# Performance work log

Measured on AMD Instinct MI355X. Metric: run time of the kernel, lower is better.

## Reference

```python
import jax, jax.numpy as jnp
import numpy as np

N, E = 20000, 320000
IN_DIM, EDGE_DIM, HID = 64, 16, 64
# (in_c, heads, channels, out_c) per layer; last layer heads=1, concat=False
DIMS = [(64, 4, 64, 256), (256, 4, 64, 256), (256, 1, 64, 64)]


def _ln(x, g, b):
    m = x.mean(-1, keepdims=True)
    v = x.var(-1, keepdims=True)
    return (x - m) / jnp.sqrt(v + 1e-5) * g + b


def _gatv2(x, ei, ea, Wl, bl, Wr, br, We, att, bc, concat):
    # PyG GATv2Conv, eval mode (no dropout), add_self_loops=True, fill_value='mean'
    n = x.shape[0]
    H, C = att.shape
    ar = jnp.arange(n, dtype=ei.dtype)
    src = jnp.concatenate([ei[0], ar])
    dst = jnp.concatenate([ei[1], ar])
    ea_f = jnp.concatenate([ea, jnp.broadcast_to(ea.mean(0), (n, ea.shape[1]))], 0)
    xl = (x @ Wl + bl).reshape(n, H, C)   # source transform
    xr = (x @ Wr + br).reshape(n, H, C)   # target transform
    ee = (ea_f @ We).reshape(-1, H, C)    # edge transform (no bias in PyG)
    e = jax.nn.leaky_relu(xl[src] + xr[dst] + ee, 0.2)       # [E+N, H, C]
    score = jnp.einsum('ehc,hc->eh', e, att)                 # [E+N, H]
    mx = jax.ops.segment_max(score, dst, num_segments=n)
    a = jnp.exp(score - mx[dst])
    a = a / (jax.ops.segment_sum(a, dst, num_segments=n)[dst] + 1e-16)
    out = jax.ops.segment_sum(a[:, :, None] * xl[src], dst, num_segments=n)  # [N,H,C]
    out = out.reshape(n, H * C) if concat else out.mean(1)
    return out + bc


def _forward(x, eis, eas, Wp, bp, gp, bep, layers):
    h = jax.nn.gelu(_ln(x @ Wp + bp, gp, bep), approximate=False)
    for i in range(3):
        Wl, bl, Wr, br, We, att, bc, g, be, Wsk, bsk = layers[i]
        res = h @ Wsk + bsk
        h = _gatv2(h, eis[i], eas[i], Wl, bl, Wr, br, We, att, bc, i < 2)
        h = jax.nn.gelu(_ln(h, g, be), approximate=False) + res
    return h


def setup_inputs() -> dict:
    key = jax.random.key(0)
    ks = iter(jax.random.split(key, 64))
    rn = lambda shape, s=0.05: jax.random.normal(next(ks), shape, jnp.float32) * s
    d = {'x': jax.random.normal(next(ks), (N, IN_DIM), jnp.float32)}
    for i in range(3):
        d['ei%d' % i] = jax.random.randint(next(ks), (2, E), 0, N, jnp.int32)
        d['ea%d' % i] = jax.random.normal(next(ks), (E, EDGE_DIM), jnp.float32)
    d['Wp'] = rn((IN_DIM, HID)); d['bp'] = jnp.zeros(HID)
    d['gp'] = jnp.ones(HID); d['bep'] = jnp.zeros(HID)
    for i, (ic, H, C, oc) in enumerate(DIMS):
        hc = H * C
        d['Wl%d' % i] = rn((ic, hc)); d['bl%d' % i] = jnp.zeros(hc)
        d['Wr%d' % i] = rn((ic, hc)); d['br%d' % i] = jnp.zeros(hc)
        d['We%d' % i] = rn((EDGE_DIM, hc))
        d['att%d' % i] = rn((H, C), 0.1)
        d['bc%d' % i] = jnp.zeros(hc if i < 2 else C)
        d['g%d' % i] = jnp.ones(oc); d['be%d' % i] = jnp.zeros(oc)
        d['Wsk%d' % i] = rn((ic, oc)); d['bsk%d' % i] = jnp.zeros(oc)
    return d


def reference(x, ei0, ea0, ei1, ea1, ei2, ea2, Wp, bp, gp, bep,
              Wl0, bl0, Wr0, br0, We0, att0, bc0, g0, be0, Wsk0, bsk0,
              Wl1, bl1, Wr1, br1, We1, att1, bc1, g1, be1, Wsk1, bsk1,
              Wl2, bl2, Wr2, br2, We2, att2, bc2, g2, be2, Wsk2, bsk2):
    layers = [
        (Wl0, bl0, Wr0, br0, We0, att0, bc0, g0, be0, Wsk0, bsk0),
        (Wl1, bl1, Wr1, br1, We1, att1, bc1, g1, be1, Wsk1, bsk1),
        (Wl2, bl2, Wr2, br2, We2, att2, bc2, g2, be2, Wsk2, bsk2),
    ]
    return _forward(x, (ei0, ei1, ei2), (ea0, ea1, ea2), Wp, bp, gp, bep, layers)
```

## Files before the change

### kernel.cpp

```cpp
#include <hip/hip_runtime.h>
#include <hip/hip_bf16.h>
#include <math.h>

#define NV 20000
#define NE 320000
#define CSR_PAD 8

typedef __attribute__((ext_vector_type(8))) short bf16x8;
typedef __attribute__((ext_vector_type(4))) float f32x4;
typedef __attribute__((ext_vector_type(2))) _Float16 h2;

static __device__ __forceinline__ ushort f2b(float f) {
  __hip_bfloat16 h = __float2bfloat16(f);
  return *reinterpret_cast<ushort*>(&h);
}
static __device__ __forceinline__ float b2f(ushort u) {
  union { ushort s[2]; float f; } c;
  c.s[0] = 0; c.s[1] = u;
  return c.f;
}
static __device__ __forceinline__ ushort f2h(float f) {
  _Float16 h = (_Float16)f;
  return *reinterpret_cast<ushort*>(&h);
}
static __device__ __forceinline__ float blo(unsigned u) { return __uint_as_float(u << 16); }
static __device__ __forceinline__ float bhi(unsigned u) { return __uint_as_float(u & 0xffff0000u); }

static __device__ __forceinline__ float wave_sum64(float x) {
  x += __int_as_float(__builtin_amdgcn_update_dpp(0, __float_as_int(x), 0x111, 0xF, 0xF, true));
  x += __int_as_float(__builtin_amdgcn_update_dpp(0, __float_as_int(x), 0x112, 0xF, 0xF, true));
  x += __int_as_float(__builtin_amdgcn_update_dpp(0, __float_as_int(x), 0x114, 0xF, 0xF, true));
  x += __int_as_float(__builtin_amdgcn_update_dpp(0, __float_as_int(x), 0x118, 0xF, 0xF, true));
  x += __int_as_float(__builtin_amdgcn_update_dpp(0, __float_as_int(x), 0x142, 0xA, 0xF, true));
  x += __int_as_float(__builtin_amdgcn_update_dpp(0, __float_as_int(x), 0x143, 0xC, 0xF, true));
  return __int_as_float(__builtin_amdgcn_readlane(__float_as_int(x), 63));
}

static __device__ __forceinline__ float sum16(float x) {
  x += __int_as_float(__builtin_amdgcn_update_dpp(0, __float_as_int(x), 0x121, 0xF, 0xF, true));
  x += __int_as_float(__builtin_amdgcn_update_dpp(0, __float_as_int(x), 0x122, 0xF, 0xF, true));
  x += __int_as_float(__builtin_amdgcn_update_dpp(0, __float_as_int(x), 0x124, 0xF, 0xF, true));
  x += __int_as_float(__builtin_amdgcn_update_dpp(0, __float_as_int(x), 0x128, 0xF, 0xF, true));
  return x;
}

static __device__ __forceinline__ float dot16h(const uint4* __restrict__ E,
                                               const h2* __restrict__ Wch) {
#if __has_builtin(__builtin_amdgcn_fdot2)
  const h2* e = (const h2*)E;
  float s = 0.f;
#pragma unroll
  for (int j = 0; j < 8; ++j) s = __builtin_amdgcn_fdot2(e[j], Wch[j], s, false);
  return s;
#else
  const unsigned* u = (const unsigned*)E;
  float s = 0.f;
#pragma unroll
  for (int j = 0; j < 8; ++j) {
    union { unsigned v; h2 h; } cv; cv.v = u[j];
    s = fmaf((float)cv.h[0], (float)Wch[j][0], s);
    s = fmaf((float)cv.h[1], (float)Wch[j][1], s);
  }
  return s;
#endif
}

struct CJob { const float* src; ushort* dst; int K, M; };
struct PrepArgs {
  const int* ei[3];
  const float* ea[3];
  int* counts[3];
  float* easum[3];
  CJob jobs[9];
  const float *x, *Wp, *bp, *gp, *bep;
  ushort* h0;
};

__global__ __launch_bounds__(256) void prep_kernel(PrepArgs a) {
  const int y = blockIdx.y, t = threadIdx.x;
  if (y < 3) {
    if (blockIdx.x < 256) {
      const float4* ea4 = (const float4*)a.ea[y];
      const int cg = t & 3;
      int r = blockIdx.x * 64 + (t >> 2);
      const int rstride = 256 * 64;
      float4 s = make_float4(0.f, 0.f, 0.f, 0.f);
      for (; r < NE; r += rstride) {
        float4 v = ea4[(size_t)r * 4 + cg];
        s.x += v.x; s.y += v.y; s.z += v.z; s.w += v.w;
      }
      __shared__ float4 red4[256];
      red4[t] = s;
      __syncthreads();
      if (t < 4) {
        float4 tot = make_float4(0.f, 0.f, 0.f, 0.f);
        for (int j = t; j < 256; j += 4) {
          float4 v = red4[j];
          tot.x += v.x; tot.y += v.y; tot.z += v.z; tot.w += v.w;
        }
        atomicAdd(&a.easum[y][t * 4 + 0], tot.x);
        atomicAdd(&a.easum[y][t * 4 + 1], tot.y);
        atomicAdd(&a.easum[y][t * 4 + 2], tot.z);
        atomicAdd(&a.easum[y][t * 4 + 3], tot.w);
      }
    }
    int i = blockIdx.x * 256 + t;
    if (i < NE) atomicAdd(&a.counts[y][a.ei[y][NE + i]], 1);
  } else if (y == 3) {
#pragma unroll
    for (int j = 0; j < 9; ++j) {
      CJob jb = a.jobs[j];
      const int total = jb.M * jb.K;
      for (int i = blockIdx.x * 256 + t; i < total; i += gridDim.x * 256) {
        int m = i / jb.K, k = i - m * jb.K;
        jb.dst[i] = f2b(jb.src[(size_t)k * jb.M + m]);
      }
    }
  } else {
    int wid = t >> 6, lane = t & 63;
    for (int row = blockIdx.x * 4 + wid; row < NV; row += gridDim.x * 4) {
      float xv = a.x[(size_t)row * 64 + lane];
      float acc = a.bp[lane];
#pragma unroll
      for (int k = 0; k < 64; ++k) {
        float v = __shfl(xv, k, 64);
        acc = fmaf(v, a.Wp[k * 64 + lane], acc);
      }
      float s1 = wave_sum64(acc), s2 = wave_sum64(acc * acc);
      float mean = s1 * (1.0f / 64.0f);
      float var  = s2 * (1.0f / 64.0f) - mean * mean;
      float yv = (acc - mean) * rsqrtf(var + 1e-5f) * a.gp[lane] + a.bep[lane];
      float gel = 0.5f * yv * (1.0f + erff(yv * 0.70710678118654752f));
      a.h0[(size_t)row * 64 + lane] = f2b(gel);
    }
  }
}

__global__ __launch_bounds__(1024) void scan_kernel(
    int* __restrict__ countsA, int* __restrict__ cursorA)
{
  int* counts = countsA + blockIdx.x * (NV + 1);
  int* cursor = cursorA + blockIdx.x * NV;
  __shared__ int ws[16];
  __shared__ int wexcl[17];
  const int t = threadIdx.x, lane = t & 63, wid = t >> 6;
  const int base = t * 20;
  int v[20];
  int tot = 0;
#pragma unroll
  for (int j = 0; j < 20; ++j) {
    int i = base + j;
    v[j] = (i < NV) ? counts[i] : 0;
    tot += v[j];
  }
  int x = tot;
#pragma unroll
  for (int o = 1; o < 64; o <<= 1) {
    int yy = __shfl_up(x, o, 64);
    if (lane >= o) x += yy;
  }
  if (lane == 63) ws[wid] = x;
  __syncthreads();
  if (t == 0) {
    int r = 0;
#pragma unroll
    for (int j = 0; j < 16; ++j) { wexcl[j] = r; r += ws[j]; }
    wexcl[16] = r;
  }
  __syncthreads();
  int run = wexcl[wid] + (x - tot);
#pragma unroll
  for (int j = 0; j < 20; ++j) {
    int i = base + j;
    if (i < NV) { counts[i] = run; cursor[i] = run; }
    run += v[j];
  }
  if (t == 0) counts[NV] = wexcl[16];
}

struct G0SArgs {
  const ushort *A, *WT;
  const float *b0, *b1, *b2;
  ushort *O0, *O1; float* O2;
  int K, M1, M2, Mtot, NT;
  const int* ei[3]; const float* ea[3];
  int* cursor;
  unsigned* csr[3]; ushort* eab[3]; int HC[3];
};

__global__ __launch_bounds__(256) void gemm0_scatter_kernel(G0SArgs a) {
  __shared__ ushort As[128][40];
  __shared__ ushort Bs[64][40];
  const int t = threadIdx.x;
  if ((int)blockIdx.x < a.NT) {
    const int wave = t >> 6, lane = t & 63;
    const int mcols = a.Mtot >> 6;
    const int col0 = ((int)blockIdx.x % mcols) * 64, row0 = ((int)blockIdx.x / mcols) * 128;
    const int m_ = lane & 15, q = lane >> 4;
    f32x4 acc[2][4];
#pragma unroll
    for (int i = 0; i < 2; ++i)
#pragma unroll
      for (int j = 0; j < 4; ++j) acc[i][j] = (f32x4){0.f, 0.f, 0.f, 0.f};
    const int ar = t >> 1, ac = (t & 1) * 16;
    const int br = t >> 2, bcol = (t & 3) * 8;
    const ushort* Ap = a.A + (size_t)(row0 + ar) * a.K + ac;
    const ushort* Bp = a.WT + (size_t)(col0 + br) * a.K + bcol;
    const bool a_ok = (row0 + ar) < NV;
    for (int k0 = 0; k0 < a.K; k0 += 32) {
      uint4 av0 = make_uint4(0, 0, 0, 0), av1 = make_uint4(0, 0, 0, 0);
      if (a_ok) { av0 = *(const uint4*)(Ap + k0); av1 = *(const uint4*)(Ap + k0 + 8); }
      uint4 bv = *(const uint4*)(Bp + k0);
      *(uint4*)&As[ar][ac] = av0;
      *(uint4*)&As[ar][ac + 8] = av1;
      *(uint4*)&Bs[br][bcol] = bv;
      __syncthreads();
      bf16x8 a0 = *(const bf16x8*)&As[wave * 32 + m_][q * 8];
      bf16x8 a1 = *(const bf16x8*)&As[wave * 32 + 16 + m_][q * 8];
#pragma unroll
      for (int cf = 0; cf < 4; ++cf) {
        bf16x8 b = *(const bf16x8*)&Bs[cf * 16 + m_][q * 8];
        acc[0][cf] = __builtin_amdgcn_mfma_f32_16x16x32_bf16(a0, b, acc[0][cf], 0, 0, 0);
        acc[1][cf] = __builtin_amdgcn_mfma_f32_16x16x32_bf16(a1, b, acc[1][cf], 0, 0, 0);
      }
      __syncthreads();
    }
    const float* bias; int base, mode, Wd;
    if (col0 < a.M1)      { bias = a.b0; base = 0;    mode = 0; Wd = a.M1; }
    else if (col0 < a.M2) { bias = a.b1; base = a.M1; mode = 1; Wd = a.M2 - a.M1; }
    else                  { bias = a.b2; base = a.M2; mode = 2; Wd = a.Mtot - a.M2; }
#pragma unroll
    for (int rf = 0; rf < 2; ++rf) {
#pragma unroll
      for (int cf = 0; cf < 4; ++cf) {
        int col = col0 + cf * 16 + m_ - base;
        float bb = bias[col];
#pragma unroll
        for (int r = 0; r < 4; ++r) {
          int row = row0 + wave * 32 + rf * 16 + q * 4 + r;
          if (row < NV) {
            float v = acc[rf][cf][r] + bb;
            if (mode == 0)      a.O0[(size_t)row * Wd + col] = f2b(v);
            else if (mode == 1) a.O1[(size_t)row * Wd + col] = f2b(v);
            else                a.O2[(size_t)row * Wd + col] = v;
          }
        }
      }
    }
  } else {
    const int per = NE + CSR_PAD;
    int gi = ((int)blockIdx.x - a.NT) * 256 + t;
    if (gi >= 3 * per) return;
    int l = gi / per, i = gi - l * per;
    if (i >= NE) {
      a.csr[l][i] = 0u;
      uint4 z = make_uint4(0, 0, 0, 0);
      *(uint4*)(a.eab[l] + (size_t)i * 16) = z;
      *(uint4*)(a.eab[l] + (size_t)i * 16 + 8) = z;
      return;
    }
    int dst = a.ei[l][NE + i], src = a.ei[l][i];
    int pos = atomicAdd(&a.cursor[(size_t)l * NV + dst], 1);
    a.csr[l][pos] = (unsigned)(src * a.HC[l]);
    const float4* er = (const float4*)(a.ea[l] + (size_t)i * 16);
    float4 q0 = er[0], q1 = er[1], q2 = er[2], q3 = er[3];
    uint4 w0, w1;
    w0.x = (unsigned)f2h(q0.x) | ((unsigned)f2h(q0.y) << 16);
    w0.y = (unsigned)f2h(q0.z) | ((unsigned)f2h(q0.w) << 16);
    w0.z = (unsigned)f2h(q1.x) | ((unsigned)f2h(q1.y) << 16);
    w0.w = (unsigned)f2h(q1.z) | ((unsigned)f2h(q1.w) << 16);
    w1.x = (unsigned)f2h(q2.x) | ((unsigned)f2h(q2.y) << 16);
    w1.y = (unsigned)f2h(q2.z) | ((unsigned)f2h(q2.w) << 16);
    w1.z = (unsigned)f2h(q3.x) | ((unsigned)f2h(q3.y) << 16);
    w1.w = (unsigned)f2h(q3.z) | ((unsigned)f2h(q3.w) << 16);
    *(uint4*)(a.eab[l] + (size_t)pos * 16) = w0;
    *(uint4*)(a.eab[l] + (size_t)pos * 16 + 8) = w1;
  }
}

__global__ __launch_bounds__(256) void gemm_fused(
    const ushort* __restrict__ A, const ushort* __restrict__ WT,
    const float* __restrict__ b0, const float* __restrict__ b1,
    const float* __restrict__ b2,
    ushort* __restrict__ O0, ushort* __restrict__ O1, float* __restrict__ O2,
    int N, int K, int M1, int M2, int Mtot)
{
  __shared__ ushort As[128][40];
  __shared__ ushort Bs[64][40];
  const int t = threadIdx.x, wave = t >> 6, lane = t & 63;
  const int row0 = blockIdx.y * 128, col0 = blockIdx.x * 64;
  const int m_ = lane & 15, q = lane >> 4;
  f32x4 acc[2][4];
#pragma unroll
  for (int i = 0; i < 2; ++i)
#pragma unroll
    for (int j = 0; j < 4; ++j) acc[i][j] = (f32x4){0.f, 0.f, 0.f, 0.f};
  const int ar = t >> 1, ac = (t & 1) * 16;
  const int br = t >> 2, bcol = (t & 3) * 8;
  const ushort* Ap = A + (size_t)(row0 + ar) * K + ac;
  const ushort* Bp = WT + (size_t)(col0 + br) * K + bcol;
  const bool a_ok = (row0 + ar) < N;
  for (int k0 = 0; k0 < K; k0 += 32) {
    uint4 av0 = make_uint4(0, 0, 0, 0), av1 = make_uint4(0, 0, 0, 0);
    if (a_ok) { av0 = *(const uint4*)(Ap + k0); av1 = *(const uint4*)(Ap + k0 + 8); }
    uint4 bv = *(const uint4*)(Bp + k0);
    *(uint4*)&As[ar][ac] = av0;
    *(uint4*)&As[ar][ac + 8] = av1;
    *(uint4*)&Bs[br][bcol] = bv;
    __syncthreads();
    bf16x8 a0 = *(const bf16x8*)&As[wave * 32 + m_][q * 8];
    bf16x8 a1 = *(const bf16x8*)&As[wave * 32 + 16 + m_][q * 8];
#pragma unroll
    for (int cf = 0; cf < 4; ++cf) {
      bf16x8 b = *(const bf16x8*)&Bs[cf * 16 + m_][q * 8];
      acc[0][cf] = __builtin_amdgcn_mfma_f32_16x16x32_bf16(a0, b, acc[0][cf], 0, 0, 0);
      acc[1][cf] = __builtin_amdgcn_mfma_f32_16x16x32_bf16(a1, b, acc[1][cf], 0, 0, 0);
    }
    __syncthreads();
  }
  const float* bias; int base, mode, Wd;
  if (col0 < M1)      { bias = b0; base = 0;  mode = 0; Wd = M1; }
  else if (col0 < M2) { bias = b1; base = M1; mode = 1; Wd = M2 - M1; }
  else                { bias = b2; base = M2; mode = 2; Wd = Mtot - M2; }
#pragma unroll
  for (int rf = 0; rf < 2; ++rf) {
#pragma unroll
    for (int cf = 0; cf < 4; ++cf) {
      int col = col0 + cf * 16 + m_ - base;
      float bb = bias[col];
#pragma unroll
      for (int r = 0; r < 4; ++r) {
        int row = row0 + wave * 32 + rf * 16 + q * 4 + r;
        if (row < N) {
          float v = acc[rf][cf][r] + bb;
          if (mode == 0)      O0[(size_t)row * Wd + col] = f2b(v);
          else if (mode == 1) O1[(size_t)row * Wd + col] = f2b(v);
          else                O2[(size_t)row * Wd + col] = v;
        }
      }
    }
  }
}

__global__ __launch_bounds__(256) void agg4_kernel(
    const ushort* __restrict__ eab, const float* __restrict__ easum,
    const float* __restrict__ We,
    const ushort* __restrict__ xl, const ushort* __restrict__ xr,
    const float* __restrict__ att, const float* __restrict__ bc,
    const float* __restrict__ g, const float* __restrict__ be,
    const float* __restrict__ res,
    const int* __restrict__ offs, const unsigned* __restrict__ csr,
    ushort* __restrict__ houtb, int E)
{
  const int t = threadIdx.x, lane = t & 63, wave = t >> 6;
  const int n = blockIdx.x * 4 + wave;
  const int cb = 4 * lane;
  const size_t rowb = (size_t)n * 256 + cb;
  const float L2E = 1.4426950408889634f;

  float4 atv = *(const float4*)(att + cb);
  float at[4] = {atv.x * L2E, atv.y * L2E, atv.z * L2E, atv.w * L2E};

  h2 Wch[4][8];
  float esf[4] = {0.f, 0.f, 0.f, 0.f};
#pragma unroll
  for (int k = 0; k < 8; ++k) {
    float4 wr0 = *(const float4*)(We + (2 * k) * 256 + cb);
    float4 wr1 = *(const float4*)(We + (2 * k + 1) * 256 + cb);
    const float* w0 = &wr0.x;
    const float* w1 = &wr1.x;
    float e0 = easum[2 * k], e1 = easum[2 * k + 1];
#pragma unroll
    for (int j = 0; j < 4; ++j) {
      esf[j] = fmaf(e0, w0[j], esf[j]);
      esf[j] = fmaf(e1, w1[j], esf[j]);
      Wch[j][k] = (h2){(_Float16)w0[j], (_Float16)w1[j]};
    }
  }
#pragma unroll
  for (int j = 0; j < 4; ++j) esf[j] *= 1.0f / (float)E;

  uint2 qr = *(const uint2*)(xr + rowb);
  float xrv[4] = {blo(qr.x), bhi(qr.x), blo(qr.y), bhi(qr.y)};
  uint2 qn = *(const uint2*)(xl + rowb);
  float xln[4] = {blo(qn.x), bhi(qn.x), blo(qn.y), bhi(qn.y)};

  float p = 0.f;
#pragma unroll
  for (int j = 0; j < 4; ++j) {
    float v = xln[j] + xrv[j] + esf[j];
    v = v > 0.f ? v : 0.2f * v;
    p = fmaf(v, at[j], p);
  }
  float wself = exp2f(sum16(p));
  float acc[4];
#pragma unroll
  for (int j = 0; j < 4; ++j) acc[j] = wself * xln[j];
  float denom = wself;

  const int beg = __builtin_amdgcn_readfirstlane(offs[n]);
  const int end = __builtin_amdgcn_readfirstlane(offs[n + 1]);

  unsigned P[2];
  uint4 EA[2][2];
  uint2 XL[2];
#pragma unroll
  for (int k = 0; k < 2; ++k) {
    P[k] = csr[beg + k];
    const uint4* ep = (const uint4*)(eab + (size_t)(beg + k) * 16);
    EA[k][0] = ep[0]; EA[k][1] = ep[1];
  }
#pragma unroll
  for (int k = 0; k < 2; ++k)
    XL[k] = *(const uint2*)(xl + __builtin_amdgcn_readfirstlane(P[k]) + cb);

  for (int idx = beg; idx < end; idx += 2) {
    unsigned Q[2];
    uint4 EB[2][2];
    uint2 XN[2];
#pragma unroll
    for (int k = 0; k < 2; ++k) Q[k] = csr[idx + 2 + k];
#pragma unroll
    for (int k = 0; k < 2; ++k) {
      const uint4* ep = (const uint4*)(eab + (size_t)(idx + 2 + k) * 16);
      EB[k][0] = ep[0]; EB[k][1] = ep[1];
    }
#pragma unroll
    for (int k = 0; k < 2; ++k)
      XN[k] = *(const uint2*)(xl + __builtin_amdgcn_readfirstlane(Q[k]) + cb);

#pragma unroll
    for (int k = 0; k < 2; ++k) {
      float xf[4] = {blo(XL[k].x), bhi(XL[k].x), blo(XL[k].y), bhi(XL[k].y)};
      float pp = 0.f;
#pragma unroll
      for (int j = 0; j < 4; ++j) {
        float ee = dot16h(EA[k], Wch[j]);
        float v = xf[j] + xrv[j] + ee;
        v = v > 0.f ? v : 0.2f * v;
        pp = fmaf(v, at[j], pp);
      }
      float S = sum16(pp);
      float w = (idx + k < end) ? exp2f(S) : 0.f;
#pragma unroll
      for (int j = 0; j < 4; ++j) acc[j] = fmaf(w, xf[j], acc[j]);
      denom += w;
    }
#pragma unroll
    for (int k = 0; k < 2; ++k) { P[k] = Q[k]; EA[k][0] = EB[k][0]; EA[k][1] = EB[k][1]; XL[k] = XN[k]; }
  }

  const float inv = 1.0f / (denom + 1e-16f);
  float4 bcv = *(const float4*)(bc + cb);
  float out[4];
  out[0] = acc[0] * inv + bcv.x; out[1] = acc[1] * inv + bcv.y;
  out[2] = acc[2] * inv + bcv.z; out[3] = acc[3] * inv + bcv.w;

  float so1 = out[0] + out[1] + out[2] + out[3];
  float so2 = out[0] * out[0] + out[1] * out[1] + out[2] * out[2] + out[3] * out[3];
  float s1 = wave_sum64(so1), s2 = wave_sum64(so2);
  float mean = s1 * (1.0f / 256.0f);
  float var  = s2 * (1.0f / 256.0f) - mean * mean;
  float rstd = rsqrtf(var + 1e-5f);
  float4 gv = *(const float4*)(g + cb);
  float4 bev = *(const float4*)(be + cb);
  float4 rv = *(const float4*)(res + rowb);
  const float* gp = &gv.x; const float* bep = &bev.x; const float* rp = &rv.x;
  ushort ob[4];
#pragma unroll
  for (int j = 0; j < 4; ++j) {
    float y = (out[j] - mean) * rstd * gp[j] + bep[j];
    float gel = 0.5f * y * (1.0f + erff(y * 0.70710678118654752f));
    ob[j] = f2b(gel + rp[j]);
  }
  uint2 ov;
  ov.x = (unsigned)ob[0] | ((unsigned)ob[1] << 16);
  ov.y = (unsigned)ob[2] | ((unsigned)ob[3] << 16);
  *(uint2*)(houtb + rowb) = ov;
}

__global__ __launch_bounds__(256, 4) void agg1_kernel(
    const ushort* __restrict__ eab, const float* __restrict__ easum,
    const float* __restrict__ We,
    const ushort* __restrict__ xl, const ushort* __restrict__ xr,
    const float* __restrict__ att, const float* __restrict__ bc,
    const float* __restrict__ g, const float* __restrict__ be,
    const float* __restrict__ res,
    const int* __restrict__ offs, const unsigned* __restrict__ csr,
    float* __restrict__ houtf, int E)
{
  const int HC = 64;
  const int t = threadIdx.x, lane = t & 63, wave = t >> 6;
  const int n = blockIdx.x * 4 + wave;
  const int c = lane;

  const float xr_t = b2f(xr[(size_t)n * HC + c]);
  const float att_t = att[c] * 1.4426950408889634f;
  float eself = 0.f;
  h2 Wch[8];
#pragma unroll
  for (int j = 0; j < 8; ++j) {
    float w0 = We[(2 * j) * HC + c], w1 = We[(2 * j + 1) * HC + c];
    eself = fmaf(easum[2 * j], w0, eself);
    eself = fmaf(easum[2 * j + 1], w1, eself);
    Wch[j] = (h2){(_Float16)w0, (_Float16)w1};
  }
  eself *= 1.0f / (float)E;

  const float xln = b2f(xl[(size_t)n * HC + c]);
  float vs = xln + xr_t + eself;
  vs = vs > 0.f ? vs : 0.2f * vs;
  const float wself = exp2f(wave_sum64(vs * att_t));
  float acc = wself * xln, denom = wself;

  const int beg = __builtin_amdgcn_readfirstlane(offs[n]);
  const int end = __builtin_amdgcn_readfirstlane(offs[n + 1]);

  unsigned P[4];
  uint4 EA[4][2];
  float XL[4];
#pragma unroll
  for (int k = 0; k < 4; ++k) {
    P[k] = csr[beg + k];
    const uint4* ep = (const uint4*)(eab + (size_t)(beg + k) * 16);
    EA[k][0] = ep[0]; EA[k][1] = ep[1];
  }
#pragma unroll
  for (int k = 0; k < 4; ++k)
    XL[k] = b2f(xl[__builtin_amdgcn_readfirstlane(P[k]) + c]);

  for (int idx = beg; idx < end; idx += 4) {
    unsigned Q[4];
    uint4 EB[4][2];
    float XLN[4];
#pragma unroll
    for (int k = 0; k < 4; ++k) Q[k] = csr[idx + 4 + k];
#pragma unroll
    for (int k = 0; k < 4; ++k) {
      const uint4* ep = (const uint4*)(eab + (size_t)(idx + 4 + k) * 16);
      EB[k][0] = ep[0]; EB[k][1] = ep[1];
    }
#pragma unroll
    for (int k = 0; k < 4; ++k)
      XLN[k] = b2f(xl[__builtin_amdgcn_readfirstlane(Q[k]) + c]);

    float wv[4];
#pragma unroll
    for (int k = 0; k < 4; ++k) {
      float ee = dot16h(EA[k], Wch);
      float v = XL[k] + xr_t + ee;
      v = v > 0.f ? v : 0.2f * v;
      float S = wave_sum64(v * att_t);
      wv[k] = (idx + k < end) ? exp2f(S) : 0.f;
    }
#pragma unroll
    for (int k = 0; k < 4; ++k) { acc = fmaf(wv[k], XL[k], acc); denom += wv[k]; }
#pragma unroll
    for (int k = 0; k < 4; ++k) {
      P[k] = Q[k]; EA[k][0] = EB[k][0]; EA[k][1] = EB[k][1]; XL[k] = XLN[k];
    }
  }

  float out = acc / (denom + 1e-16f) + bc[c];
  float s1 = wave_sum64(out), s2 = wave_sum64(out * out);
  float mean = s1 / (float)HC;
  float var  = s2 / (float)HC - mean * mean;
  float y = (out - mean) * rsqrtf(var + 1e-5f) * g[c] + be[c];
  float gel = 0.5f * y * (1.0f + erff(y * 0.70710678118654752f));
  houtf[(size_t)n * HC + c] = gel + res[(size_t)n * HC + c];
}

extern "C" void kernel_launch(void* const* d_in, const int* in_sizes, int n_in,
                              void* d_out, int out_size, void* d_ws, size_t ws_size,
                              hipStream_t stream)
{
  auto in = [&](int i) { return (const float*)d_in[i]; };

  const int ic[3] = {64, 256, 256}, hc[3] = {256, 256, 64}, oc[3] = {256, 256, 64};
  const int CSRN = NE + CSR_PAD;

  char* w = (char*)d_ws;
  size_t off = 0;
  auto alloc = [&](size_t bytes) { void* p = w + off; off = (off + bytes + 511) & ~(size_t)511; return p; };
  ushort* B1   = (ushort*)alloc((size_t)NV * 256 * 2);
  ushort* B2   = (ushort*)alloc((size_t)NV * 256 * 2);
  float*  B3   = (float*)alloc((size_t)NV * 256 * 4);
  ushort* h0bf = (ushort*)alloc((size_t)NV * 64 * 2);
  ushort* h1bf = (ushort*)alloc((size_t)NV * 256 * 2);
  ushort* h2bf = (ushort*)alloc((size_t)NV * 256 * 2);
  ushort* Wcat[3];
  for (int i = 0; i < 3; ++i)
    Wcat[i] = (ushort*)alloc((size_t)(2 * hc[i] + oc[i]) * ic[i] * 2);
  float*    easumA  = (float*)alloc(3 * 64);
  int*      countsA = (int*)alloc((size_t)3 * (NV + 1) * 4);
  int*      cursorA = (int*)alloc((size_t)3 * NV * 4);
  unsigned* csrA    = (unsigned*)alloc((size_t)3 * CSRN * 4);
  ushort*   eabA    = (ushort*)alloc((size_t)3 * CSRN * 16 * 2);

  hipMemsetAsync(easumA, 0, 512 + (size_t)3 * (NV + 1) * 4, stream);

  PrepArgs pa;
  for (int i = 0; i < 3; ++i) {
    pa.ei[i] = (const int*)d_in[1 + 2 * i];
    pa.ea[i] = in(2 + 2 * i);
    pa.counts[i] = countsA + i * (NV + 1);
    pa.easum[i] = easumA + i * 16;
    pa.jobs[i * 3 + 0] = {in(11 + 11 * i), Wcat[i],                             ic[i], hc[i]};
    pa.jobs[i * 3 + 1] = {in(13 + 11 * i), Wcat[i] + (size_t)hc[i] * ic[i],     ic[i], hc[i]};
    pa.jobs[i * 3 + 2] = {in(20 + 11 * i), Wcat[i] + (size_t)2 * hc[i] * ic[i], ic[i], oc[i]};
  }
  pa.x = in(0); pa.Wp = in(7); pa.bp = in(8); pa.gp = in(9); pa.bep = in(10);
  pa.h0 = h0bf;
  prep_kernel<<<dim3(1344, 5), 256, 0, stream>>>(pa);

  scan_kernel<<<3, 1024, 0, stream>>>(countsA, cursorA);

  G0SArgs ga;
  ga.A = h0bf; ga.WT = Wcat[0];
  ga.b0 = in(12); ga.b1 = in(14); ga.b2 = in(21);
  ga.O0 = B1; ga.O1 = B2; ga.O2 = B3;
  ga.K = 64; ga.M1 = 256; ga.M2 = 512; ga.Mtot = 768;
  ga.NT = (768 / 64) * ((NV + 127) / 128);
  for (int i = 0; i < 3; ++i) {
    ga.ei[i] = (const int*)d_in[1 + 2 * i];
    ga.ea[i] = in(2 + 2 * i);
    ga.csr[i] = csrA + (size_t)i * CSRN;
    ga.eab[i] = eabA + (size_t)i * CSRN * 16;
    ga.HC[i] = hc[i];
  }
  ga.cursor = cursorA;
  const int scat_blocks = (3 * (NE + CSR_PAD) + 255) / 256;
  gemm0_scatter_kernel<<<ga.NT + scat_blocks, 256, 0, stream>>>(ga);

  agg4_kernel<<<NV / 4, 256, 0, stream>>>(
      eabA + 0, easumA + 0, in(15), B1, B2, in(16), in(17), in(18), in(19),
      B3, countsA, csrA, h1bf, NE);

  gemm_fused<<<dim3(768 / 64, (NV + 127) / 128), 256, 0, stream>>>(
      h1bf, Wcat[1], in(23), in(25), in(32), B1, B2, B3, NV, 256, 256, 512, 768);

  agg4_kernel<<<NV / 4, 256, 0, stream>>>(
      eabA + (size_t)CSRN * 16, easumA + 16, in(26), B1, B2, in(27), in(28),
      in(29), in(30), B3, countsA + (NV + 1), csrA + (size_t)CSRN, h2bf, NE);

  gemm_fused<<<dim3(192 / 64, (NV + 127) / 128), 256, 0, stream>>>(
      h2bf, Wcat[2], in(34), in(36), in(43), B1, B2, B3, NV, 256, 64, 128, 192);

  agg1_kernel<<<NV / 4, 256, 0, stream>>>(
      eabA + (size_t)2 * CSRN * 16, easumA + 32, in(37), B1, B2, in(38), in(39),
      in(40), in(41), B3, countsA + 2 * (NV + 1), csrA + (size_t)2 * CSRN,
      (float*)d_out, NE);
}
```

Before: 539.4 us.

## Rebalance preprocessing kernels: split histogram, merge scan with projection, move easum

Preprocessing is regrouped into new launches. The degree histogram gets its own kernel. The prefix scan runs alongside the weight transpose, CSR padding zeroing and input projection in one kernel of 1024-thread blocks. The edge-attribute mean reduction moves into the layer-0 GEMM/scatter kernel. Offsets now go to a separate buffer so scan output no longer overwrites counts. The aim is to cut the serial critical path and let the long-latency reductions overlap with the GEMM, in exchange for an extra buffer and heavier mixed-role kernels.

```diff
diff --git a/kernel.cpp b/kernel.cpp
--- a/kernel.cpp
+++ b/kernel.cpp
@@ -4,7 +4,7 @@
 
 #define NV 20000
 #define NE 320000
-#define CSR_PAD 8
+#define CSR_PAD 16
 
 typedef __attribute__((ext_vector_type(8))) short bf16x8;
 typedef __attribute__((ext_vector_type(4))) float f32x4;
@@ -65,120 +65,101 @@
 #endif
 }
 
+struct HArgs { const int* ei[3]; int* counts; };
+
+__global__ __launch_bounds__(256) void hist_kernel(HArgs a) {
+  int gi = blockIdx.x * 256 + threadIdx.x;
+  int l = gi / NE, i = gi - l * NE;
+  atomicAdd(&a.counts[(size_t)l * (NV + 1) + a.ei[l][NE + i]], 1);
+}
+
 struct CJob { const float* src; ushort* dst; int K, M; };
-struct PrepArgs {
-  const int* ei[3];
-  const float* ea[3];
-  int* counts[3];
-  float* easum[3];
+struct K2Args {
+  const int* counts; int* offs; int* cursor;
   CJob jobs[9];
+  unsigned* csr[3]; ushort* eab[3];
   const float *x, *Wp, *bp, *gp, *bep;
   ushort* h0;
 };
 
-__global__ __launch_bounds__(256) void prep_kernel(PrepArgs a) {
-  const int y = blockIdx.y, t = threadIdx.x;
-  if (y < 3) {
-    if (blockIdx.x < 256) {
-      const float4* ea4 = (const float4*)a.ea[y];
-      const int cg = t & 3;
-      int r = blockIdx.x * 64 + (t >> 2);
-      const int rstride = 256 * 64;
-      float4 s = make_float4(0.f, 0.f, 0.f, 0.f);
-      for (; r < NE; r += rstride) {
-        float4 v = ea4[(size_t)r * 4 + cg];
-        s.x += v.x; s.y += v.y; s.z += v.z; s.w += v.w;
-      }
-      __shared__ float4 red4[256];
-      red4[t] = s;
-      __syncthreads();
-      if (t < 4) {
-        float4 tot = make_float4(0.f, 0.f, 0.f, 0.f);
-        for (int j = t; j < 256; j += 4) {
-          float4 v = red4[j];
-          tot.x += v.x; tot.y += v.y; tot.z += v.z; tot.w += v.w;
-        }
-        atomicAdd(&a.easum[y][t * 4 + 0], tot.x);
-        atomicAdd(&a.easum[y][t * 4 + 1], tot.y);
-        atomicAdd(&a.easum[y][t * 4 + 2], tot.z);
-        atomicAdd(&a.easum[y][t * 4 + 3], tot.w);
-      }
-    }
-    int i = blockIdx.x * 256 + t;
-    if (i < NE) atomicAdd(&a.counts[y][a.ei[y][NE + i]], 1);
-  } else if (y == 3) {
+__global__ __launch_bounds__(1024) void scan_proj_kernel(K2Args a) {
+  const int b = blockIdx.x, t = threadIdx.x;
+  if (b < 3) {
+    const int* counts = a.counts + b * (NV + 1);
+    int* offs = a.offs + b * (NV + 1);
+    int* cursor = a.cursor + b * NV;
+    __shared__ int ws[16];
+    __shared__ int wexcl[17];
+    const int lane = t & 63, wid = t >> 6;
+    const int base = t * 20;
+    int v[20];
+    int tot = 0;
+#pragma unroll
+    for (int j = 0; j < 20; ++j) {
+      int i = base + j;
+      v[j] = (i < NV) ? counts[i] : 0;
+      tot += v[j];
+    }
+    int x = tot;
+#pragma unroll
+    for (int o = 1; o < 64; o <<= 1) {
+      int yy = __shfl_up(x, o, 64);
+      if (lane >= o) x += yy;
+    }
+    if (lane == 63) ws[wid] = x;
+    __syncthreads();
+    if (t == 0) {
+      int r = 0;
+#pragma unroll
+      for (int j = 0; j < 16; ++j) { wexcl[j] = r; r += ws[j]; }
+      wexcl[16] = r;
+    }
+    __syncthreads();
+    int run = wexcl[wid] + (x - tot);
+#pragma unroll
+    for (int j = 0; j < 20; ++j) {
+      int i = base + j;
+      if (i < NV) { offs[i] = run; cursor[i] = run; }
+      run += v[j];
+    }
+    if (t == 0) offs[NV] = wexcl[16];
+  } else if (b < 19) {
+    if (b == 3 && t < 3 * CSR_PAD) {
+      int l = t >> 4, p = t & 15;
+      a.csr[l][NE + p] = 0u;
+      uint4 z = make_uint4(0, 0, 0, 0);
+      *(uint4*)(a.eab[l] + (size_t)(NE + p) * 16) = z;
+      *(uint4*)(a.eab[l] + (size_t)(NE + p) * 16 + 8) = z;
+    }
 #pragma unroll
     for (int j = 0; j < 9; ++j) {
       CJob jb = a.jobs[j];
       const int total = jb.M * jb.K;
-      for (int i = blockIdx.x * 256 + t; i < total; i += gridDim.x * 256) {
+      for (int i = (b - 3) * 1024 + t; i < total; i += 16 * 1024) {
         int m = i / jb.K, k = i - m * jb.K;
         jb.dst[i] = f2b(jb.src[(size_t)k * jb.M + m]);
       }
     }
   } else {
-    int wid = t >> 6, lane = t & 63;
-    for (int row = blockIdx.x * 4 + wid; row < NV; row += gridDim.x * 4) {
-      float xv = a.x[(size_t)row * 64 + lane];
-      float acc = a.bp[lane];
-#pragma unroll
-      for (int k = 0; k < 64; ++k) {
-        float v = __shfl(xv, k, 64);
-        acc = fmaf(v, a.Wp[k * 64 + lane], acc);
-      }
-      float s1 = wave_sum64(acc), s2 = wave_sum64(acc * acc);
-      float mean = s1 * (1.0f / 64.0f);
-      float var  = s2 * (1.0f / 64.0f) - mean * mean;
-      float yv = (acc - mean) * rsqrtf(var + 1e-5f) * a.gp[lane] + a.bep[lane];
-      float gel = 0.5f * yv * (1.0f + erff(yv * 0.70710678118654752f));
-      a.h0[(size_t)row * 64 + lane] = f2b(gel);
-    }
-  }
-}
-
-__global__ __launch_bounds__(1024) void scan_kernel(
-    int* __restrict__ countsA, int* __restrict__ cursorA)
-{
-  int* counts = countsA + blockIdx.x * (NV + 1);
-  int* cursor = cursorA + blockIdx.x * NV;
-  __shared__ int ws[16];
-  __shared__ int wexcl[17];
-  const int t = threadIdx.x, lane = t & 63, wid = t >> 6;
-  const int base = t * 20;
-  int v[20];
-  int tot = 0;
-#pragma unroll
-  for (int j = 0; j < 20; ++j) {
-    int i = base + j;
-    v[j] = (i < NV) ? counts[i] : 0;
-    tot += v[j];
-  }
-  int x = tot;
-#pragma unroll
-  for (int o = 1; o < 64; o <<= 1) {
-    int yy = __shfl_up(x, o, 64);
-    if (lane >= o) x += yy;
-  }
-  if (lane == 63) ws[wid] = x;
-  __syncthreads();
-  if (t == 0) {
-    int r = 0;
-#pragma unroll
-    for (int j = 0; j < 16; ++j) { wexcl[j] = r; r += ws[j]; }
-    wexcl[16] = r;
-  }
-  __syncthreads();
-  int run = wexcl[wid] + (x - tot);
-#pragma unroll
-  for (int j = 0; j < 20; ++j) {
-    int i = base + j;
-    if (i < NV) { counts[i] = run; cursor[i] = run; }
-    run += v[j];
-  }
-  if (t == 0) counts[NV] = wexcl[16];
-}
-
-struct G0SArgs {
+    const int wid = t >> 6, lane = t & 63;
+    const int row = (b - 19) * 16 + wid;
+    float xv = a.x[(size_t)row * 64 + lane];
+    float acc = a.bp[lane];
+#pragma unroll
+    for (int k = 0; k < 64; ++k) {
+      float v = __shfl(xv, k, 64);
+      acc = fmaf(v, a.Wp[k * 64 + lane], acc);
+    }
+    float s1 = wave_sum64(acc), s2 = wave_sum64(acc * acc);
+    float mean = s1 * (1.0f / 64.0f);
+    float var  = s2 * (1.0f / 64.0f) - mean * mean;
+    float yv = (acc - mean) * rsqrtf(var + 1e-5f) * a.gp[lane] + a.bep[lane];
+    float gel = 0.5f * yv * (1.0f + erff(yv * 0.70710678118654752f));
+    a.h0[(size_t)row * 64 + lane] = f2b(gel);
+  }
+}
+
+struct K3Args {
   const ushort *A, *WT;
   const float *b0, *b1, *b2;
   ushort *O0, *O1; float* O2;
@@ -186,16 +167,18 @@
   const int* ei[3]; const float* ea[3];
   int* cursor;
   unsigned* csr[3]; ushort* eab[3]; int HC[3];
+  float* easum[3];
 };
 
-__global__ __launch_bounds__(256) void gemm0_scatter_kernel(G0SArgs a) {
+__global__ __launch_bounds__(256) void mega_kernel(K3Args a) {
   __shared__ ushort As[128][40];
   __shared__ ushort Bs[64][40];
   const int t = threadIdx.x;
-  if ((int)blockIdx.x < a.NT) {
+  const int b = (int)blockIdx.x;
+  if (b < a.NT) {
     const int wave = t >> 6, lane = t & 63;
     const int mcols = a.Mtot >> 6;
-    const int col0 = ((int)blockIdx.x % mcols) * 64, row0 = ((int)blockIdx.x / mcols) * 128;
+    const int col0 = (b % mcols) * 64, row0 = (b / mcols) * 128;
     const int m_ = lane & 15, q = lane >> 4;
     f32x4 acc[2][4];
 #pragma unroll
@@ -219,9 +202,9 @@
       bf16x8 a1 = *(const bf16x8*)&As[wave * 32 + 16 + m_][q * 8];
 #pragma unroll
       for (int cf = 0; cf < 4; ++cf) {
-        bf16x8 b = *(const bf16x8*)&Bs[cf * 16 + m_][q * 8];
-        acc[0][cf] = __builtin_amdgcn_mfma_f32_16x16x32_bf16(a0, b, acc[0][cf], 0, 0, 0);
-        acc[1][cf] = __builtin_amdgcn_mfma_f32_16x16x32_bf16(a1, b, acc[1][cf], 0, 0, 0);
+        bf16x8 bfr = *(const bf16x8*)&Bs[cf * 16 + m_][q * 8];
+        acc[0][cf] = __builtin_amdgcn_mfma_f32_16x16x32_bf16(a0, bfr, acc[0][cf], 0, 0, 0);
+        acc[1][cf] = __builtin_amdgcn_mfma_f32_16x16x32_bf16(a1, bfr, acc[1][cf], 0, 0, 0);
       }
       __syncthreads();
     }
@@ -247,18 +230,9 @@
         }
       }
     }
-  } else {
-    const int per = NE + CSR_PAD;
-    int gi = ((int)blockIdx.x - a.NT) * 256 + t;
-    if (gi >= 3 * per) return;
-    int l = gi / per, i = gi - l * per;
-    if (i >= NE) {
-      a.csr[l][i] = 0u;
-      uint4 z = make_uint4(0, 0, 0, 0);
-      *(uint4*)(a.eab[l] + (size_t)i * 16) = z;
-      *(uint4*)(a.eab[l] + (size_t)i * 16 + 8) = z;
-      return;
-    }
+  } else if (b < a.NT + 3750) {
+    int gi = (b - a.NT) * 256 + t;
+    int l = gi / NE, i = gi - l * NE;
     int dst = a.ei[l][NE + i], src = a.ei[l][i];
     int pos = atomicAdd(&a.cursor[(size_t)l * NV + dst], 1);
     a.csr[l][pos] = (unsigned)(src * a.HC[l]);
@@ -275,6 +249,32 @@
     w1.w = (unsigned)f2h(q3.z) | ((unsigned)f2h(q3.w) << 16);
     *(uint4*)(a.eab[l] + (size_t)pos * 16) = w0;
     *(uint4*)(a.eab[l] + (size_t)pos * 16 + 8) = w1;
+  } else {
+    const int cb = b - a.NT - 3750;
+    const int l = cb >> 8, blk = cb & 255;
+    const float4* ea4 = (const float4*)a.ea[l];
+    const int cg = t & 3;
+    int r = blk * 64 + (t >> 2);
+    const int rstride = 256 * 64;
+    float4 s = make_float4(0.f, 0.f, 0.f, 0.f);
+    for (; r < NE; r += rstride) {
+      float4 v = ea4[(size_t)r * 4 + cg];
+      s.x += v.x; s.y += v.y; s.z += v.z; s.w += v.w;
+    }
+    float4* red4 = (float4*)&As[0][0];
+    red4[t] = s;
+    __syncthreads();
+    if (t < 4) {
+      float4 tot = make_float4(0.f, 0.f, 0.f, 0.f);
+      for (int j = t; j < 256; j += 4) {
+        float4 v = red4[j];
+        tot.x += v.x; tot.y += v.y; tot.z += v.z; tot.w += v.w;
+      }
+      atomicAdd(&a.easum[l][t * 4 + 0], tot.x);
+      atomicAdd(&a.easum[l][t * 4 + 1], tot.y);
+      atomicAdd(&a.easum[l][t * 4 + 2], tot.z);
+      atomicAdd(&a.easum[l][t * 4 + 3], tot.w);
+    }
   }
 }
 
@@ -312,9 +312,9 @@
     bf16x8 a1 = *(const bf16x8*)&As[wave * 32 + 16 + m_][q * 8];
 #pragma unroll
     for (int cf = 0; cf < 4; ++cf) {
-      bf16x8 b = *(const bf16x8*)&Bs[cf * 16 + m_][q * 8];
-      acc[0][cf] = __builtin_amdgcn_mfma_f32_16x16x32_bf16(a0, b, acc[0][cf], 0, 0, 0);
-      acc[1][cf] = __builtin_amdgcn_mfma_f32_16x16x32_bf16(a1, b, acc[1][cf], 0, 0, 0);
+      bf16x8 bfr = *(const bf16x8*)&Bs[cf * 16 + m_][q * 8];
+      acc[0][cf] = __builtin_amdgcn_mfma_f32_16x16x32_bf16(a0, bfr, acc[0][cf], 0, 0, 0);
+      acc[1][cf] = __builtin_amdgcn_mfma_f32_16x16x32_bf16(a1, bfr, acc[1][cf], 0, 0, 0);
     }
     __syncthreads();
   }
@@ -593,29 +593,32 @@
     Wcat[i] = (ushort*)alloc((size_t)(2 * hc[i] + oc[i]) * ic[i] * 2);
   float*    easumA  = (float*)alloc(3 * 64);
   int*      countsA = (int*)alloc((size_t)3 * (NV + 1) * 4);
+  int*      offsA   = (int*)alloc((size_t)3 * (NV + 1) * 4);
   int*      cursorA = (int*)alloc((size_t)3 * NV * 4);
   unsigned* csrA    = (unsigned*)alloc((size_t)3 * CSRN * 4);
   ushort*   eabA    = (ushort*)alloc((size_t)3 * CSRN * 16 * 2);
 
   hipMemsetAsync(easumA, 0, 512 + (size_t)3 * (NV + 1) * 4, stream);
 
-  PrepArgs pa;
+  HArgs ha;
+  for (int i = 0; i < 3; ++i) ha.ei[i] = (const int*)d_in[1 + 2 * i];
+  ha.counts = countsA;
+  hist_kernel<<<3 * NE / 256, 256, 0, stream>>>(ha);
+
+  K2Args k2;
+  k2.counts = countsA; k2.offs = offsA; k2.cursor = cursorA;
   for (int i = 0; i < 3; ++i) {
-    pa.ei[i] = (const int*)d_in[1 + 2 * i];
-    pa.ea[i] = in(2 + 2 * i);
-    pa.counts[i] = countsA + i * (NV + 1);
-    pa.easum[i] = easumA + i * 16;
-    pa.jobs[i * 3 + 0] = {in(11 + 11 * i), Wcat[i],                             ic[i], hc[i]};
-    pa.jobs[i * 3 + 1] = {in(13 + 11 * i), Wcat[i] + (size_t)hc[i] * ic[i],     ic[i], hc[i]};
-    pa.jobs[i * 3 + 2] = {in(20 + 11 * i), Wcat[i] + (size_t)2 * hc[i] * ic[i], ic[i], oc[i]};
-  }
-  pa.x = in(0); pa.Wp = in(7); pa.bp = in(8); pa.gp = in(9); pa.bep = in(10);
-  pa.h0 = h0bf;
-  prep_kernel<<<dim3(1344, 5), 256, 0, stream>>>(pa);
-
-  scan_kernel<<<3, 1024, 0, stream>>>(countsA, cursorA);
-
-  G0SArgs ga;
+    k2.jobs[i * 3 + 0] = {in(11 + 11 * i), Wcat[i],                             ic[i], hc[i]};
+    k2.jobs[i * 3 + 1] = {in(13 + 11 * i), Wcat[i] + (size_t)hc[i] * ic[i],     ic[i], hc[i]};
+    k2.jobs[i * 3 + 2] = {in(20 + 11 * i), Wcat[i] + (size_t)2 * hc[i] * ic[i], ic[i], oc[i]};
+    k2.csr[i] = csrA + (size_t)i * CSRN;
+    k2.eab[i] = eabA + (size_t)i * CSRN * 16;
+  }
+  k2.x = in(0); k2.Wp = in(7); k2.bp = in(8); k2.gp = in(9); k2.bep = in(10);
+  k2.h0 = h0bf;
+  scan_proj_kernel<<<19 + NV / 16, 1024, 0, stream>>>(k2);
+
+  K3Args ga;
   ga.A = h0bf; ga.WT = Wcat[0];
   ga.b0 = in(12); ga.b1 = in(14); ga.b2 = in(21);
   ga.O0 = B1; ga.O1 = B2; ga.O2 = B3;
@@ -627,27 +630,27 @@
     ga.csr[i] = csrA + (size_t)i * CSRN;
     ga.eab[i] = eabA + (size_t)i * CSRN * 16;
     ga.HC[i] = hc[i];
+    ga.easum[i] = easumA + i * 16;
   }
   ga.cursor = cursorA;
-  const int scat_blocks = (3 * (NE + CSR_PAD) + 255) / 256;
-  gemm0_scatter_kernel<<<ga.NT + scat_blocks, 256, 0, stream>>>(ga);
+  mega_kernel<<<ga.NT + 3750 + 768, 256, 0, stream>>>(ga);
 
   agg4_kernel<<<NV / 4, 256, 0, stream>>>(
       eabA + 0, easumA + 0, in(15), B1, B2, in(16), in(17), in(18), in(19),
-      B3, countsA, csrA, h1bf, NE);
+      B3, offsA, csrA, h1bf, NE);
 
   gemm_fused<<<dim3(768 / 64, (NV + 127) / 128), 256, 0, stream>>>(
       h1bf, Wcat[1], in(23), in(25), in(32), B1, B2, B3, NV, 256, 256, 512, 768);
 
   agg4_kernel<<<NV / 4, 256, 0, stream>>>(
       eabA + (size_t)CSRN * 16, easumA + 16, in(26), B1, B2, in(27), in(28),
-      in(29), in(30), B3, countsA + (NV + 1), csrA + (size_t)CSRN, h2bf, NE);
+      in(29), in(30), B3, offsA + (NV + 1), csrA + (size_t)CSRN, h2bf, NE);
 
   gemm_fused<<<dim3(192 / 64, (NV + 127) / 128), 256, 0, stream>>>(
       h2bf, Wcat[2], in(34), in(36), in(43), B1, B2, B3, NV, 256, 64, 128, 192);
 
   agg1_kernel<<<NV / 4, 256, 0, stream>>>(
       eabA + (size_t)2 * CSRN * 16, easumA + 32, in(37), B1, B2, in(38), in(39),
-      in(40), in(41), B3, countsA + 2 * (NV + 1), csrA + (size_t)2 * CSRN,
+      in(40), in(41), B3, offsA + 2 * (NV + 1), csrA + (size_t)2 * CSRN,
       (float*)d_out, NE);
 }
```

Result: no change. 543.7 us (+0.8%).
